# Optimization experiments

Measured on AMD Instinct MI355X. Metric: run time of the kernel, lower is better.

Reference implementation:

```python
import jax, jax.numpy as jnp
import numpy as np

NUM_CLASSES = 21
THRESHOLD = 0.5
VAR0, VAR1 = 0.1, 0.2
NEGPOS_RATIO = 3


def setup_inputs() -> dict:
    key = jax.random.key(0)
    k1, k2, k3, k4, k5, k6, k7 = jax.random.split(key, 7)
    B, P, C, O = 64, 8732, 21, 8
    loc_data = jax.random.normal(k1, (B, P, 4), dtype=jnp.float32) * 0.1
    conf_data = jax.random.normal(k2, (B, P, C), dtype=jnp.float32)
    # priors: center form (cx, cy, w, h), valid in [0,1]
    cxy = jax.random.uniform(k3, (P, 2), minval=0.05, maxval=0.95)
    pwh = jax.random.uniform(k4, (P, 2), minval=0.05, maxval=0.3)
    priors = jnp.concatenate([cxy, pwh], axis=-1).astype(jnp.float32)
    # targets: corner-form boxes + class label (float), (B, O, 5)
    tc = jax.random.uniform(k5, (B, O, 2), minval=0.2, maxval=0.8)
    twh = jax.random.uniform(k6, (B, O, 2), minval=0.1, maxval=0.4)
    tmin = jnp.clip(tc - twh / 2, 0.0, 1.0)
    tmax = jnp.clip(tc + twh / 2, 0.0, 1.0)
    labels = jax.random.randint(k7, (B, O, 1), 0, C - 1).astype(jnp.float32)
    targets = jnp.concatenate([tmin, tmax, labels], axis=-1)
    return {"loc_data": loc_data, "conf_data": conf_data, "priors": priors, "targets": targets}


def _point_form(p):
    # (cx,cy,w,h) -> (xmin,ymin,xmax,ymax)
    return jnp.concatenate([p[:, :2] - p[:, 2:] / 2, p[:, :2] + p[:, 2:] / 2], axis=-1)


def _jaccard(a, b):
    # a: (O,4) corners, b: (P,4) corners -> (O,P)
    lt = jnp.maximum(a[:, None, :2], b[None, :, :2])
    rb = jnp.minimum(a[:, None, 2:], b[None, :, 2:])
    wh = jnp.clip(rb - lt, 0.0, None)
    inter = wh[..., 0] * wh[..., 1]
    area_a = ((a[:, 2] - a[:, 0]) * (a[:, 3] - a[:, 1]))[:, None]
    area_b = ((b[:, 2] - b[:, 0]) * (b[:, 3] - b[:, 1]))[None, :]
    return inter / (area_a + area_b - inter)


def _match_one(truths, labels, priors_pt, priors):
    # truths: (O,4) corners, labels: (O,), priors: (P,4) center-form
    ov = _jaccard(truths, priors_pt)                      # (O,P)
    best_prior_idx = jnp.argmax(ov, axis=1)               # (O,)
    best_truth_overlap = jnp.max(ov, axis=0)              # (P,)
    best_truth_idx = jnp.argmax(ov, axis=0)               # (P,)
    # ensure every gt box matches its best prior
    best_truth_overlap = best_truth_overlap.at[best_prior_idx].set(2.0)
    best_truth_idx = best_truth_idx.at[best_prior_idx].set(jnp.arange(truths.shape[0]))
    matched = truths[best_truth_idx]                      # (P,4)
    conf = labels[best_truth_idx].astype(jnp.int32) + 1
    conf = jnp.where(best_truth_overlap < THRESHOLD, 0, conf)
    # encode offsets
    g_cxcy = ((matched[:, :2] + matched[:, 2:]) / 2 - priors[:, :2]) / (VAR0 * priors[:, 2:])
    g_wh = jnp.log(jnp.clip((matched[:, 2:] - matched[:, :2]) / priors[:, 2:], 1e-8, None)) / VAR1
    return jnp.concatenate([g_cxcy, g_wh], axis=-1), conf


def _forward(loc_data, conf_data, priors, targets):
    B, P, C = conf_data.shape
    priors_sg = jax.lax.stop_gradient(priors)             # torch uses .data
    targets_sg = jax.lax.stop_gradient(targets)
    priors_pt = _point_form(priors_sg)
    loc_t, conf_t = jax.vmap(_match_one, in_axes=(0, 0, None, None))(
        targets_sg[:, :, :4], targets_sg[:, :, 4], priors_pt, priors_sg)
    pos = conf_t > 0                                      # (B,P)

    # localization: smooth L1 summed over positive priors
    diff = loc_data - loc_t
    ad = jnp.abs(diff)
    sl1 = jnp.where(ad < 1.0, 0.5 * diff * diff, ad - 0.5)
    loss_l = jnp.sum(sl1 * pos[..., None].astype(sl1.dtype))

    # per-prior conf loss for hard negative mining
    lse = jax.nn.logsumexp(conf_data, axis=-1)            # (B,P)
    gathered = jnp.take_along_axis(conf_data, conf_t[..., None], axis=-1)[..., 0]
    loss_c_all = lse - gathered                           # (B,P)
    mined = jnp.where(pos, 0.0, loss_c_all)
    loss_idx = jnp.argsort(-mined, axis=1)                # descending
    idx_rank = jnp.argsort(loss_idx, axis=1)
    num_pos = jnp.sum(pos.astype(jnp.int32), axis=1, keepdims=True)  # (B,1)
    num_neg = jnp.minimum(NEGPOS_RATIO * num_pos, P - num_pos)
    neg = idx_rank < num_neg                              # (B,P)

    sel = (pos | neg).astype(loss_c_all.dtype)
    loss_c = jnp.sum(loss_c_all * sel)

    N = jnp.sum(num_pos).astype(loss_l.dtype)
    return loss_l / N, loss_c / N


def reference(loc_data, conf_data, priors, targets):
    return _forward(loc_data, conf_data, priors, targets)
```

## Files before the change

### kernel.cpp

```cpp
#include <hip/hip_runtime.h>
#include <math.h>

#define TPB 256
#define TPBS 1024
#define NVREG 9

typedef unsigned long long ull;
typedef float pf4 __attribute__((ext_vector_type(4), aligned(4)));

__device__ __forceinline__ float jac(float tx0, float ty0, float tx1, float ty1, float ta,
                                     float px0, float py0, float px1, float py1, float pa) {
    float ltx = fmaxf(tx0, px0), lty = fmaxf(ty0, py0);
    float rbx = fminf(tx1, px1), rby = fminf(ty1, py1);
    float w = fmaxf(rbx - ltx, 0.0f), h = fmaxf(rby - lty, 0.0f);
    float inter = w * h;
    return inter / (ta + pa - inter);
}

template <int ON, int CN>
__global__ __launch_bounds__(TPB) void fused_kernel(
    const float* __restrict__ loc, const float* __restrict__ priors,
    const float* __restrict__ targets, const float* __restrict__ conf,
    int P, int O_rt, int C_rt, int CB2,
    float* __restrict__ mined, ull* __restrict__ pkeys,
    float* __restrict__ part_ll, float* __restrict__ part_pc,
    int* __restrict__ part_np, unsigned* __restrict__ chist) {
    constexpr int OMAX = (ON > 0) ? ON : 64;
    constexpr int CC = (CN > 0) ? CN : 32;
    constexpr int WPB = TPB / 64;
    const int O = (ON > 0) ? ON : O_rt;
    const int C = (CN > 0) ? CN : C_rt;
    const int b = blockIdx.x / CB2;
    const int chunk = blockIdx.x % CB2;
    const int tid = threadIdx.x;
    const int p = chunk * TPB + tid;
    const bool pv = (p < P);
    const int lane = tid & 63, wv = tid >> 6;
    const int CB2W = CB2 * WPB;

    __shared__ float s_tx0[OMAX], s_ty0[OMAX], s_tx1[OMAX], s_ty1[OMAX];
    __shared__ float s_lab[OMAX], s_area[OMAX];
    __shared__ int s_h[256];
    __shared__ float s_wll[WPB], s_wpc[WPB];
    __shared__ int s_wnp[WPB];

    float rv[CC];
    float4 pr4 = make_float4(0.f, 0.f, 1.f, 1.f);
    if (pv) {
        const float* row = conf + ((size_t)b * P + p) * C;
        if (CN > 0) {
#pragma unroll
            for (int q = 0; q < CN / 4; ++q) {
                pf4 v = *(const pf4*)(row + 4 * q);
#pragma unroll
                for (int e = 0; e < 4; ++e) rv[4 * q + e] = v[e];
            }
#pragma unroll
            for (int j = (CN / 4) * 4; j < CN; ++j) rv[j] = row[j];
        } else {
            for (int j = 0; j < C; ++j) rv[j] = row[j];
        }
        pr4 = ((const float4*)priors)[p];
    }

    s_h[tid] = 0;
    for (int o = tid; o < O; o += TPB) {
        const float* t = targets + ((size_t)b * O + o) * 5;
        float x0 = t[0], y0 = t[1], x1 = t[2], y1 = t[3];
        s_tx0[o] = x0; s_ty0[o] = y0; s_tx1[o] = x1; s_ty1[o] = y1;
        s_lab[o] = t[4];
        s_area[o] = (x1 - x0) * (y1 - y0);
    }
    __syncthreads();

    float cx = pr4.x, cy = pr4.y, pw = pr4.z, ph = pr4.w;
    float px0 = cx - pw * 0.5f, py0 = cy - ph * 0.5f;
    float px1 = cx + pw * 0.5f, py1 = cy + ph * 0.5f;
    float pa = (px1 - px0) * (py1 - py0);
    float bto = -1.0f;
    int bti = 0;
    for (int o = 0; o < O; ++o) {
        float ov = -1.0f;
        if (pv) {
            ov = jac(s_tx0[o], s_ty0[o], s_tx1[o], s_ty1[o], s_area[o],
                     px0, py0, px1, py1, pa);
            if (ov > bto) { bto = ov; bti = o; }
        }
        float mx = ov;
#pragma unroll
        for (int d = 1; d < 64; d <<= 1)
            mx = fmaxf(mx, __shfl_xor(mx, d, 64));
        ull kk = 0ull;
        if (mx >= 0.0f) {
            ull msk = __ballot(ov == mx);
            int src = __ffsll(msk) - 1;
            unsigned pw_ = (unsigned)(chunk * TPB + (wv << 6) + src);
            kk = ((ull)__float_as_uint(mx) << 32) | (ull)(0xFFFFFFFFu - pw_);
        }
        if (lane == 0)
            pkeys[((size_t)b * O + o) * CB2W + chunk * WPB + wv] = kk;
    }

    float ll = 0.0f, pc = 0.0f;
    int np = 0;
    int bin = 0;
    bool hv = false;
    if (pv) {
        float m = rv[0];
#pragma unroll
        for (int j = 1; j < CC; ++j) { if (CN > 0 || j < C) m = fmaxf(m, rv[j]); }
        float s = 0.0f;
#pragma unroll
        for (int j = 0; j < CC; ++j) { if (CN > 0 || j < C) s += __expf(rv[j] - m); }
        float lse = m + __logf(s);

        int c = (bto < 0.5f) ? 0 : ((int)s_lab[bti] + 1);
        float rowc = rv[0];
#pragma unroll
        for (int j = 1; j < CC; ++j) { if (CN > 0 || j < C) { if (c == j) rowc = rv[j]; } }
        float lc = lse - rowc;

        bool pos = c > 0;
        float mv = pos ? 0.0f : lc;
        mined[(size_t)b * P + p] = mv;
        bin = (int)(__float_as_uint(mv) >> 24);
        hv = true;
        if (pos) {
            pc = lc;
            np = 1;
            float mx0 = s_tx0[bti], my0 = s_ty0[bti];
            float mx1 = s_tx1[bti], my1 = s_ty1[bti];
            float g0 = ((mx0 + mx1) * 0.5f - cx) / (0.1f * pw);
            float g1 = ((my0 + my1) * 0.5f - cy) / (0.1f * ph);
            float g2 = logf(fmaxf((mx1 - mx0) / pw, 1e-8f)) / 0.2f;
            float g3 = logf(fmaxf((my1 - my0) / ph, 1e-8f)) / 0.2f;
            float4 ld = ((const float4*)loc)[(size_t)b * P + p];
            float gt4[4] = {g0, g1, g2, g3};
            float lv[4] = {ld.x, ld.y, ld.z, ld.w};
#pragma unroll
            for (int q = 0; q < 4; ++q) {
                float d = lv[q] - gt4[q];
                float ad = fabsf(d);
                ll += (ad < 1.0f) ? 0.5f * d * d : (ad - 0.5f);
            }
        }
    }

    {
        ull act = __ballot(hv);
        while (act) {
            int src = __ffsll(act) - 1;
            int b0 = __shfl(bin, src, 64);
            ull same = __ballot(hv && bin == b0) & act;
            if (lane == src) atomicAdd(&s_h[b0], (int)__popcll(same));
            act &= ~same;
        }
    }

#pragma unroll
    for (int d = 1; d < 64; d <<= 1) {
        ll += __shfl_xor(ll, d, 64);
        pc += __shfl_xor(pc, d, 64);
        np += __shfl_xor(np, d, 64);
    }
    if (lane == 0) { s_wll[wv] = ll; s_wpc[wv] = pc; s_wnp[wv] = np; }
    __syncthreads();
    if (tid == 0) {
        float L = 0.f, Pc = 0.f;
        int N = 0;
        for (int w = 0; w < WPB; ++w) { L += s_wll[w]; Pc += s_wpc[w]; N += s_wnp[w]; }
        part_ll[blockIdx.x] = L;
        part_pc[blockIdx.x] = Pc;
        part_np[blockIdx.x] = N;
    }
    if (tid < 128) {
        unsigned wd = (unsigned)s_h[2 * tid] | ((unsigned)s_h[2 * tid + 1] << 16);
        chist[((size_t)b * CB2 + chunk) * 128 + tid] = wd;
    }
}

template <int ON, int CN>
__global__ __launch_bounds__(TPBS) void select_kernel(
    const float* __restrict__ mined, const float* __restrict__ conf,
    const float* __restrict__ loc, const float* __restrict__ priors,
    const float* __restrict__ targets, const ull* __restrict__ pkeys,
    const float* __restrict__ part_ll, const float* __restrict__ part_pc,
    const int* __restrict__ part_np, const unsigned* __restrict__ chist,
    float* __restrict__ ll_batch, float* __restrict__ lc_batch,
    int* __restrict__ np_batch,
    int P, int O_rt, int C_rt, int CB2, int ratio) {
    constexpr int OMAX = (ON > 0) ? ON : 64;
    constexpr int NV = NVREG;
    const int O = (ON > 0) ? ON : O_rt;
    const int C = (CN > 0) ? CN : C_rt;
    const int b = blockIdx.x, tid = threadIdx.x;
    const int lane = tid & 63, wv = tid >> 6;
    constexpr int W = TPBS / 64;
    const int CB2W = CB2 * (TPB / 64);
    const float* v = mined + (size_t)b * P;
    const bool reg = (P <= NV * TPBS);

    __shared__ int s_hist[256];
    __shared__ float s_tx0[OMAX], s_ty0[OMAX], s_tx1[OMAX], s_ty1[OMAX];
    __shared__ float s_lab[OMAX], s_area[OMAX];
    __shared__ ull s_keys[OMAX];
    __shared__ int s_bp[OMAX];
    __shared__ float s_wf[W], s_wg[W];
    __shared__ int s_wi[W];
    __shared__ int s_wt[4];
    __shared__ unsigned s_bsel;
    __shared__ int s_krn;
    __shared__ float s_bc[2], s_fix[2];
    __shared__ int s_bn, s_fixn;

    float val[NV];
#pragma unroll
    for (int j = 0; j < NV; ++j) {
        int i = tid + j * TPBS;
        val[j] = (reg && i < P) ? v[i] : 0.0f;
    }

    float pll = 0.0f, ppc = 0.0f;
    int pnp = 0;
    for (int i = tid; i < CB2; i += TPBS) {
        pll += part_ll[b * CB2 + i];
        ppc += part_pc[b * CB2 + i];
        pnp += part_np[b * CB2 + i];
    }
#pragma unroll
    for (int d = 1; d < 64; d <<= 1) {
        pll += __shfl_xor(pll, d, 64);
        ppc += __shfl_xor(ppc, d, 64);
        pnp += __shfl_xor(pnp, d, 64);
    }
    if (lane == 0) { s_wf[wv] = pll; s_wg[wv] = ppc; s_wi[wv] = pnp; }

    if (tid < O) {
        const float* t = targets + ((size_t)b * O + tid) * 5;
        float x0 = t[0], y0 = t[1], x1 = t[2], y1 = t[3];
        s_tx0[tid] = x0; s_ty0[tid] = y0; s_tx1[tid] = x1; s_ty1[tid] = y1;
        s_lab[tid] = t[4];
        s_area[tid] = (x1 - x0) * (y1 - y0);
        s_keys[tid] = 0ull;
    }
    __syncthreads();

    for (int i = tid; i < O * CB2W; i += TPBS) {
        int o = i / CB2W, s = i % CB2W;
        atomicMax(&s_keys[o], pkeys[((size_t)b * O + o) * CB2W + s]);
    }
    __syncthreads();
    if (tid < O)
        s_bp[tid] = (int)(0xFFFFFFFFu - (unsigned)(s_keys[tid] & 0xFFFFFFFFull));
    __syncthreads();

    if (reg) {
#pragma unroll
        for (int j = 0; j < NV; ++j) {
            int i = tid + j * TPBS;
            bool z = false;
            for (int o = 0; o < O; ++o) z |= (s_bp[o] == i);
            if (z) val[j] = 0.0f;
        }
    }
    unsigned uvv[NV];
#pragma unroll
    for (int j = 0; j < NV; ++j) uvv[j] = __float_as_uint(val[j]);

    if (tid < 256) {
        int h = 0;
        const unsigned* cb = chist + (size_t)b * CB2 * 128 + (tid >> 1);
        const int sh = (tid & 1) * 16;
        for (int c = 0; c < CB2; ++c) h += (int)((cb[c * 128] >> sh) & 0xFFFFu);
        s_hist[tid] = h;
    }

    float dll = 0.0f, dpc = 0.0f;
    int dnp = 0;
    int adj_bin = -1;
    if (tid < O) {
        const int o = tid;
        const int p = s_bp[o];
        bool owner = true;
        for (int o2 = o + 1; o2 < O; ++o2)
            if (s_bp[o2] == p) owner = false;
        if (owner) {
            adj_bin = (int)(__float_as_uint(v[p]) >> 24);
            float4 pr = ((const float4*)priors)[p];
            float cx = pr.x, cy = pr.y, pw = pr.z, ph = pr.w;
            float px0 = cx - pw * 0.5f, py0 = cy - ph * 0.5f;
            float px1 = cx + pw * 0.5f, py1 = cy + ph * 0.5f;
            float pa = (px1 - px0) * (py1 - py0);
            float bto = -1.0f;
            int bti = 0;
            for (int o2 = 0; o2 < O; ++o2) {
                float ov = jac(s_tx0[o2], s_ty0[o2], s_tx1[o2], s_ty1[o2], s_area[o2],
                               px0, py0, px1, py1, pa);
                if (ov > bto) { bto = ov; bti = o2; }
            }
            int c_t = (bto < 0.5f) ? 0 : ((int)s_lab[bti] + 1);
            const float* row = conf + ((size_t)b * P + p) * C;
            float m = row[0];
            for (int j = 1; j < C; ++j) m = fmaxf(m, row[j]);
            float s = 0.0f;
            for (int j = 0; j < C; ++j) s += __expf(row[j] - m);
            float lse = m + __logf(s);
            int c_n = (int)s_lab[o] + 1;
            float lc_n = lse - row[c_n];
            bool pos_t = c_t > 0;
            float lc_t = lse - row[c_t];
            dpc = lc_n - (pos_t ? lc_t : 0.0f);
            dnp = 1 - (pos_t ? 1 : 0);
            float4 ld = ((const float4*)loc)[(size_t)b * P + p];
            float lv[4] = {ld.x, ld.y, ld.z, ld.w};
            float sl_new = 0.0f, sl_old = 0.0f;
            {
                float mx0 = s_tx0[o], my0 = s_ty0[o], mx1 = s_tx1[o], my1 = s_ty1[o];
                float g[4] = {((mx0 + mx1) * 0.5f - cx) / (0.1f * pw),
                              ((my0 + my1) * 0.5f - cy) / (0.1f * ph),
                              logf(fmaxf((mx1 - mx0) / pw, 1e-8f)) / 0.2f,
                              logf(fmaxf((my1 - my0) / ph, 1e-8f)) / 0.2f};
                for (int q = 0; q < 4; ++q) {
                    float d = lv[q] - g[q];
                    float ad = fabsf(d);
                    sl_new += (ad < 1.0f) ? 0.5f * d * d : (ad - 0.5f);
                }
            }
            if (pos_t) {
                float mx0 = s_tx0[bti], my0 = s_ty0[bti], mx1 = s_tx1[bti], my1 = s_ty1[bti];
                float g[4] = {((mx0 + mx1) * 0.5f - cx) / (0.1f * pw),
                              ((my0 + my1) * 0.5f - cy) / (0.1f * ph),
                              logf(fmaxf((mx1 - mx0) / pw, 1e-8f)) / 0.2f,
                              logf(fmaxf((my1 - my0) / ph, 1e-8f)) / 0.2f};
                for (int q = 0; q < 4; ++q) {
                    float d = lv[q] - g[q];
                    float ad = fabsf(d);
                    sl_old += (ad < 1.0f) ? 0.5f * d * d : (ad - 0.5f);
                }
            }
            dll = sl_new - sl_old;
        }
    }
    if (wv == 0) {
#pragma unroll
        for (int d = 1; d < 64; d <<= 1) {
            dll += __shfl_xor(dll, d, 64);
            dpc += __shfl_xor(dpc, d, 64);
            dnp += __shfl_xor(dnp, d, 64);
        }
        if (lane == 0) { s_fix[0] = dll; s_fix[1] = dpc; s_fixn = dnp; }
    }
    __syncthreads();
    if (adj_bin > 0) {
        atomicAdd(&s_hist[adj_bin], -1);
        atomicAdd(&s_hist[0], 1);
    }
    if (tid == 0) {
        float L = 0.f, Pc = 0.f;
        int N = 0;
        for (int w = 0; w < W; ++w) { L += s_wf[w]; Pc += s_wg[w]; N += s_wi[w]; }
        s_bc[0] = L + s_fix[0]; s_bc[1] = Pc + s_fix[1]; s_bn = N + s_fixn;
    }
    __syncthreads();
    const float ll_sum = s_bc[0];
    const float sum_pos = s_bc[1];
    const int npos = s_bn;

    const int k = min(ratio * npos, P - npos);
    if (tid == 0) {
        ll_batch[b] = ll_sum;
        np_batch[b] = npos;
    }
    if (k <= 0) {
        if (tid == 0) lc_batch[b] = sum_pos;
        return;
    }

    unsigned prefix = 0u;
    int kr = k;
    for (int pass = 0; pass < 4; ++pass) {
        const int shift = 24 - 8 * pass;
        if (pass > 0) {
            const unsigned mask = 0xFFFFFFFFu << (32 - 8 * pass);
            if (tid < 256) s_hist[tid] = 0;
            __syncthreads();
            if (reg) {
#pragma unroll
                for (int j = 0; j < NV; ++j) {
                    int i = tid + j * TPBS;
                    unsigned u = uvv[j];
                    if (i < P && (u & mask) == prefix)
                        atomicAdd(&s_hist[(u >> shift) & 0xFF], 1);
                }
            } else {
                for (int i = tid; i < P; i += TPBS) {
                    float x = v[i];
                    for (int o = 0; o < O; ++o)
                        if (i == s_bp[o]) x = 0.0f;
                    unsigned u = __float_as_uint(x);
                    if ((u & mask) == prefix)
                        atomicAdd(&s_hist[(u >> shift) & 0xFF], 1);
                }
            }
            __syncthreads();
        }
        int sge = 0, h = 0;
        if (tid < 256) {
            h = s_hist[tid];
            int val_ = h;
#pragma unroll
            for (int d = 1; d < 64; d <<= 1) {
                int t = __shfl_down(val_, d, 64);
                if (lane + d < 64) val_ += t;
            }
            if (lane == 0) s_wt[tid >> 6] = val_;
            sge = val_;
        }
        __syncthreads();
        if (tid < 256) {
            for (int w = (tid >> 6) + 1; w < 4; ++w) sge += s_wt[w];
            int sgt = sge - h;
            if (sge >= kr && sgt < kr) {
                s_bsel = (unsigned)tid;
                s_krn = kr - sgt;
            }
        }
        __syncthreads();
        prefix |= s_bsel << shift;
        kr = s_krn;
    }
    const float T = __uint_as_float(prefix);
    float lsum = 0.0f;
    int lcnt = 0;
    if (reg) {
#pragma unroll
        for (int j = 0; j < NV; ++j) {
            int i = tid + j * TPBS;
            if (i < P && val[j] > T) { lsum += val[j]; ++lcnt; }
        }
    } else {
        for (int i = tid; i < P; i += TPBS) {
            float x = v[i];
            for (int o = 0; o < O; ++o)
                if (i == s_bp[o]) x = 0.0f;
            if (x > T) { lsum += x; ++lcnt; }
        }
    }
#pragma unroll
    for (int d = 1; d < 64; d <<= 1) {
        lsum += __shfl_xor(lsum, d, 64);
        lcnt += __shfl_xor(lcnt, d, 64);
    }
    if (lane == 0) { s_wf[wv] = lsum; s_wi[wv] = lcnt; }
    __syncthreads();
    if (tid == 0) {
        float S = 0.f;
        int Cn = 0;
        for (int w = 0; w < W; ++w) { S += s_wf[w]; Cn += s_wi[w]; }
        lc_batch[b] = sum_pos + S + (float)(k - Cn) * T;
    }
}

__global__ __launch_bounds__(TPB) void finalize_kernel(
    const float* __restrict__ ll_batch, const int* __restrict__ np_batch,
    const float* __restrict__ lc_batch, int B, float* __restrict__ out) {
    const int tid = threadIdx.x;
    __shared__ float s_l[TPB], s_c[TPB];
    __shared__ int s_n[TPB];
    float l = 0.0f, c = 0.0f;
    int n = 0;
    for (int i = tid; i < B; i += TPB) {
        l += ll_batch[i];
        c += lc_batch[i];
        n += np_batch[i];
    }
    s_l[tid] = l; s_c[tid] = c; s_n[tid] = n;
    __syncthreads();
    for (int s = TPB / 2; s > 0; s >>= 1) {
        if (tid < s) {
            s_l[tid] += s_l[tid + s];
            s_c[tid] += s_c[tid + s];
            s_n[tid] += s_n[tid + s];
        }
        __syncthreads();
    }
    if (tid == 0) {
        float N = (float)s_n[0];
        out[0] = s_l[0] / N;
        out[1] = s_c[0] / N;
    }
}

extern "C" void kernel_launch(void* const* d_in, const int* in_sizes, int n_in,
                              void* d_out, int out_size, void* d_ws, size_t ws_size,
                              hipStream_t stream) {
    const float* loc = (const float*)d_in[0];
    const float* conf = (const float*)d_in[1];
    const float* priors = (const float*)d_in[2];
    const float* targets = (const float*)d_in[3];

    const int P = in_sizes[2] / 4;
    const int B = in_sizes[0] / (P * 4);
    const int C = in_sizes[1] / (in_sizes[0] / 4);
    const int O = in_sizes[3] / (B * 5);
    const size_t BP = (size_t)B * P;
    const int CB2 = (P + TPB - 1) / TPB;
    const int CB2W = CB2 * (TPB / 64);

    ull* pkeys = (ull*)d_ws;
    float* mined = (float*)(pkeys + (size_t)B * O * CB2W);
    float* part_ll = mined + BP;
    float* part_pc = part_ll + (size_t)B * CB2;
    int* part_np = (int*)(part_pc + (size_t)B * CB2);
    unsigned* chist = (unsigned*)(part_np + (size_t)B * CB2);
    float* ll_batch = (float*)(chist + (size_t)B * CB2 * 128);
    float* lc_batch = ll_batch + B;
    int* np_batch = (int*)(lc_batch + B);

    if (O == 8 && C == 21) {
        fused_kernel<8, 21><<<B * CB2, TPB, 0, stream>>>(
            loc, priors, targets, conf, P, O, C, CB2,
            mined, pkeys, part_ll, part_pc, part_np, chist);
        select_kernel<8, 21><<<B, TPBS, 0, stream>>>(
            mined, conf, loc, priors, targets, pkeys, part_ll, part_pc, part_np,
            chist, ll_batch, lc_batch, np_batch, P, O, C, CB2, 3);
    } else {
        fused_kernel<0, 0><<<B * CB2, TPB, 0, stream>>>(
            loc, priors, targets, conf, P, O, C, CB2,
            mined, pkeys, part_ll, part_pc, part_np, chist);
        select_kernel<0, 0><<<B, TPBS, 0, stream>>>(
            mined, conf, loc, priors, targets, pkeys, part_ll, part_pc, part_np,
            chist, ll_batch, lc_batch, np_batch, P, O, C, CB2, 3);
    }

    finalize_kernel<<<1, TPB, 0, stream>>>(ll_batch, np_batch, lc_batch, B,
                                           (float*)d_out);
}
```

Measured before the change: 117.9 us.

## Process four prior slots per thread with double-buffered conf row loads

Each block of the fused matching kernel now covers four strips of 256 priors, so every thread handles four priors. Each target box is read from shared memory once and reused across all four IoU computations, and the per-slot overlaps are max-reduced before the wave shuffle. Conf rows are loaded into two alternating register buffers so the next row's load overlaps the current row's log-sum-exp. The aim is fewer blocks, less per-block setup and fewer partial records for the select kernel to reduce. The cost is higher register pressure and only about two blocks per CU for a memory-bound pass, which may hurt latency hiding.

New measurement: 116.8 us. No clear change (-0.9%).

```diff
diff --git a/kernel.cpp b/kernel.cpp
--- a/kernel.cpp
+++ b/kernel.cpp
@@ -2,6 +2,7 @@
 #include <math.h>
 
 #define TPB 256
+#define SLOTS 4
 #define TPBS 1024
 #define NVREG 9
 
@@ -33,20 +34,32 @@
     const int b = blockIdx.x / CB2;
     const int chunk = blockIdx.x % CB2;
     const int tid = threadIdx.x;
-    const int p = chunk * TPB + tid;
-    const bool pv = (p < P);
+    const int base = chunk * (TPB * SLOTS);
     const int lane = tid & 63, wv = tid >> 6;
-    const int CB2W = CB2 * WPB;
+    const int CB2P = CB2 * SLOTS;
 
     __shared__ float s_tx0[OMAX], s_ty0[OMAX], s_tx1[OMAX], s_ty1[OMAX];
     __shared__ float s_lab[OMAX], s_area[OMAX];
     __shared__ int s_h[256];
-    __shared__ float s_wll[WPB], s_wpc[WPB];
-    __shared__ int s_wnp[WPB];
-
-    float rv[CC];
-    float4 pr4 = make_float4(0.f, 0.f, 1.f, 1.f);
-    if (pv) {
+    __shared__ float s_wll[WPB][SLOTS], s_wpc[WPB][SLOTS];
+    __shared__ int s_wnp[WPB][SLOTS];
+
+    int p_[SLOTS];
+    bool pv_[SLOTS];
+#pragma unroll
+    for (int s = 0; s < SLOTS; ++s) { p_[s] = base + s * TPB + tid; pv_[s] = p_[s] < P; }
+
+    float px0[SLOTS], py0[SLOTS], px1[SLOTS], py1[SLOTS], pa[SLOTS];
+#pragma unroll
+    for (int s = 0; s < SLOTS; ++s) {
+        float4 pr = pv_[s] ? ((const float4*)priors)[p_[s]] : make_float4(0.f, 0.f, 1.f, 1.f);
+        px0[s] = pr.x - pr.z * 0.5f; py0[s] = pr.y - pr.w * 0.5f;
+        px1[s] = pr.x + pr.z * 0.5f; py1[s] = pr.y + pr.w * 0.5f;
+        pa[s] = (px1[s] - px0[s]) * (py1[s] - py0[s]);
+    }
+
+    float rvA[CC], rvB[CC];
+    auto loadrow = [&](float* rv, int p) {
         const float* row = conf + ((size_t)b * P + p) * C;
         if (CN > 0) {
 #pragma unroll
@@ -60,8 +73,8 @@
         } else {
             for (int j = 0; j < C; ++j) rv[j] = row[j];
         }
-        pr4 = ((const float4*)priors)[p];
-    }
+    };
+    if (pv_[0]) loadrow(rvA, p_[0]);
 
     s_h[tid] = 0;
     for (int o = tid; o < O; o += TPB) {
@@ -73,105 +86,125 @@
     }
     __syncthreads();
 
-    float cx = pr4.x, cy = pr4.y, pw = pr4.z, ph = pr4.w;
-    float px0 = cx - pw * 0.5f, py0 = cy - ph * 0.5f;
-    float px1 = cx + pw * 0.5f, py1 = cy + ph * 0.5f;
-    float pa = (px1 - px0) * (py1 - py0);
-    float bto = -1.0f;
-    int bti = 0;
+    float bto[SLOTS];
+    int bti[SLOTS];
+#pragma unroll
+    for (int s = 0; s < SLOTS; ++s) { bto[s] = -1.0f; bti[s] = 0; }
     for (int o = 0; o < O; ++o) {
-        float ov = -1.0f;
-        if (pv) {
-            ov = jac(s_tx0[o], s_ty0[o], s_tx1[o], s_ty1[o], s_area[o],
-                     px0, py0, px1, py1, pa);
-            if (ov > bto) { bto = ov; bti = o; }
-        }
-        float mx = ov;
+        float tx0 = s_tx0[o], ty0 = s_ty0[o], tx1 = s_tx1[o], ty1 = s_ty1[o], ta = s_area[o];
+        float ov[SLOTS];
+#pragma unroll
+        for (int s = 0; s < SLOTS; ++s) {
+            ov[s] = pv_[s] ? jac(tx0, ty0, tx1, ty1, ta,
+                                 px0[s], py0[s], px1[s], py1[s], pa[s])
+                           : -1.0f;
+            if (ov[s] > bto[s]) { bto[s] = ov[s]; bti[s] = o; }
+        }
+        float mx = fmaxf(fmaxf(ov[0], ov[1]), fmaxf(ov[2], ov[3]));
 #pragma unroll
         for (int d = 1; d < 64; d <<= 1)
             mx = fmaxf(mx, __shfl_xor(mx, d, 64));
         ull kk = 0ull;
         if (mx >= 0.0f) {
-            ull msk = __ballot(ov == mx);
-            int src = __ffsll(msk) - 1;
-            unsigned pw_ = (unsigned)(chunk * TPB + (wv << 6) + src);
+            ull m0 = __ballot(ov[0] == mx);
+            int ss = 0;
+            if (!m0) { m0 = __ballot(ov[1] == mx); ss = 1; }
+            if (!m0) { m0 = __ballot(ov[2] == mx); ss = 2; }
+            if (!m0) { m0 = __ballot(ov[3] == mx); ss = 3; }
+            int src = __ffsll(m0) - 1;
+            unsigned pw_ = (unsigned)(base + ss * TPB + (wv << 6) + src);
             kk = ((ull)__float_as_uint(mx) << 32) | (ull)(0xFFFFFFFFu - pw_);
         }
         if (lane == 0)
-            pkeys[((size_t)b * O + o) * CB2W + chunk * WPB + wv] = kk;
-    }
-
-    float ll = 0.0f, pc = 0.0f;
-    int np = 0;
-    int bin = 0;
-    bool hv = false;
-    if (pv) {
-        float m = rv[0];
-#pragma unroll
-        for (int j = 1; j < CC; ++j) { if (CN > 0 || j < C) m = fmaxf(m, rv[j]); }
-        float s = 0.0f;
-#pragma unroll
-        for (int j = 0; j < CC; ++j) { if (CN > 0 || j < C) s += __expf(rv[j] - m); }
-        float lse = m + __logf(s);
-
-        int c = (bto < 0.5f) ? 0 : ((int)s_lab[bti] + 1);
-        float rowc = rv[0];
-#pragma unroll
-        for (int j = 1; j < CC; ++j) { if (CN > 0 || j < C) { if (c == j) rowc = rv[j]; } }
-        float lc = lse - rowc;
-
-        bool pos = c > 0;
-        float mv = pos ? 0.0f : lc;
-        mined[(size_t)b * P + p] = mv;
-        bin = (int)(__float_as_uint(mv) >> 24);
-        hv = true;
-        if (pos) {
-            pc = lc;
-            np = 1;
-            float mx0 = s_tx0[bti], my0 = s_ty0[bti];
-            float mx1 = s_tx1[bti], my1 = s_ty1[bti];
-            float g0 = ((mx0 + mx1) * 0.5f - cx) / (0.1f * pw);
-            float g1 = ((my0 + my1) * 0.5f - cy) / (0.1f * ph);
-            float g2 = logf(fmaxf((mx1 - mx0) / pw, 1e-8f)) / 0.2f;
-            float g3 = logf(fmaxf((my1 - my0) / ph, 1e-8f)) / 0.2f;
-            float4 ld = ((const float4*)loc)[(size_t)b * P + p];
-            float gt4[4] = {g0, g1, g2, g3};
-            float lv[4] = {ld.x, ld.y, ld.z, ld.w};
-#pragma unroll
-            for (int q = 0; q < 4; ++q) {
-                float d = lv[q] - gt4[q];
-                float ad = fabsf(d);
-                ll += (ad < 1.0f) ? 0.5f * d * d : (ad - 0.5f);
-            }
-        }
-    }
-
-    {
+            pkeys[((size_t)b * O + o) * CB2P + chunk * WPB + wv] = kk;
+    }
+
+    float ll[SLOTS], pc[SLOTS];
+    int np[SLOTS];
+    auto doSlot = [&](int s, float* rv) {
+        ll[s] = 0.0f; pc[s] = 0.0f; np[s] = 0;
+        bool hv = false;
+        int bn = 0;
+        if (pv_[s]) {
+            float m = rv[0];
+#pragma unroll
+            for (int j = 1; j < CC; ++j) { if (CN > 0 || j < C) m = fmaxf(m, rv[j]); }
+            float sm = 0.0f;
+#pragma unroll
+            for (int j = 0; j < CC; ++j) { if (CN > 0 || j < C) sm += __expf(rv[j] - m); }
+            float lse = m + __logf(sm);
+
+            int c = (bto[s] < 0.5f) ? 0 : ((int)s_lab[bti[s]] + 1);
+            float rowc = rv[0];
+#pragma unroll
+            for (int j = 1; j < CC; ++j) { if (CN > 0 || j < C) { if (c == j) rowc = rv[j]; } }
+            float lc = lse - rowc;
+
+            bool pos = c > 0;
+            float mv = pos ? 0.0f : lc;
+            mined[(size_t)b * P + p_[s]] = mv;
+            bn = (int)(__float_as_uint(mv) >> 24);
+            hv = true;
+            if (pos) {
+                pc[s] = lc;
+                np[s] = 1;
+                float4 pr = ((const float4*)priors)[p_[s]];
+                float cx = pr.x, cy = pr.y, pw = pr.z, ph = pr.w;
+                float mx0 = s_tx0[bti[s]], my0 = s_ty0[bti[s]];
+                float mx1 = s_tx1[bti[s]], my1 = s_ty1[bti[s]];
+                float g0 = ((mx0 + mx1) * 0.5f - cx) / (0.1f * pw);
+                float g1 = ((my0 + my1) * 0.5f - cy) / (0.1f * ph);
+                float g2 = logf(fmaxf((mx1 - mx0) / pw, 1e-8f)) / 0.2f;
+                float g3 = logf(fmaxf((my1 - my0) / ph, 1e-8f)) / 0.2f;
+                float4 ld = ((const float4*)loc)[(size_t)b * P + p_[s]];
+                float gt4[4] = {g0, g1, g2, g3};
+                float lv[4] = {ld.x, ld.y, ld.z, ld.w};
+#pragma unroll
+                for (int q = 0; q < 4; ++q) {
+                    float d = lv[q] - gt4[q];
+                    float ad = fabsf(d);
+                    ll[s] += (ad < 1.0f) ? 0.5f * d * d : (ad - 0.5f);
+                }
+            }
+        }
         ull act = __ballot(hv);
         while (act) {
             int src = __ffsll(act) - 1;
-            int b0 = __shfl(bin, src, 64);
-            ull same = __ballot(hv && bin == b0) & act;
+            int b0 = __shfl(bn, src, 64);
+            ull same = __ballot(hv && bn == b0) & act;
             if (lane == src) atomicAdd(&s_h[b0], (int)__popcll(same));
             act &= ~same;
         }
-    }
-
-#pragma unroll
-    for (int d = 1; d < 64; d <<= 1) {
-        ll += __shfl_xor(ll, d, 64);
-        pc += __shfl_xor(pc, d, 64);
-        np += __shfl_xor(np, d, 64);
-    }
-    if (lane == 0) { s_wll[wv] = ll; s_wpc[wv] = pc; s_wnp[wv] = np; }
-    __syncthreads();
-    if (tid == 0) {
+    };
+    if (pv_[1]) loadrow(rvB, p_[1]);
+    doSlot(0, rvA);
+    if (pv_[2]) loadrow(rvA, p_[2]);
+    doSlot(1, rvB);
+    if (pv_[3]) loadrow(rvB, p_[3]);
+    doSlot(2, rvA);
+    doSlot(3, rvB);
+
+#pragma unroll
+    for (int s = 0; s < SLOTS; ++s) {
+        float l = ll[s], q = pc[s];
+        int n = np[s];
+#pragma unroll
+        for (int d = 1; d < 64; d <<= 1) {
+            l += __shfl_xor(l, d, 64);
+            q += __shfl_xor(q, d, 64);
+            n += __shfl_xor(n, d, 64);
+        }
+        if (lane == 0) { s_wll[wv][s] = l; s_wpc[wv][s] = q; s_wnp[wv][s] = n; }
+    }
+    __syncthreads();
+    if (tid < SLOTS) {
         float L = 0.f, Pc = 0.f;
         int N = 0;
-        for (int w = 0; w < WPB; ++w) { L += s_wll[w]; Pc += s_wpc[w]; N += s_wnp[w]; }
-        part_ll[blockIdx.x] = L;
-        part_pc[blockIdx.x] = Pc;
-        part_np[blockIdx.x] = N;
+        for (int w = 0; w < WPB; ++w) { L += s_wll[w][tid]; Pc += s_wpc[w][tid]; N += s_wnp[w][tid]; }
+        int pidx = b * CB2P + chunk * SLOTS + tid;
+        part_ll[pidx] = L;
+        part_pc[pidx] = Pc;
+        part_np[pidx] = N;
     }
     if (tid < 128) {
         unsigned wd = (unsigned)s_h[2 * tid] | ((unsigned)s_h[2 * tid + 1] << 16);
@@ -196,7 +229,7 @@
     const int b = blockIdx.x, tid = threadIdx.x;
     const int lane = tid & 63, wv = tid >> 6;
     constexpr int W = TPBS / 64;
-    const int CB2W = CB2 * (TPB / 64);
+    const int CB2P = CB2 * SLOTS;
     const float* v = mined + (size_t)b * P;
     const bool reg = (P <= NV * TPBS);
 
@@ -222,10 +255,10 @@
 
     float pll = 0.0f, ppc = 0.0f;
     int pnp = 0;
-    for (int i = tid; i < CB2; i += TPBS) {
-        pll += part_ll[b * CB2 + i];
-        ppc += part_pc[b * CB2 + i];
-        pnp += part_np[b * CB2 + i];
+    for (int i = tid; i < CB2P; i += TPBS) {
+        pll += part_ll[b * CB2P + i];
+        ppc += part_pc[b * CB2P + i];
+        pnp += part_np[b * CB2P + i];
     }
 #pragma unroll
     for (int d = 1; d < 64; d <<= 1) {
@@ -245,9 +278,9 @@
     }
     __syncthreads();
 
-    for (int i = tid; i < O * CB2W; i += TPBS) {
-        int o = i / CB2W, s = i % CB2W;
-        atomicMax(&s_keys[o], pkeys[((size_t)b * O + o) * CB2W + s]);
+    for (int i = tid; i < O * CB2P; i += TPBS) {
+        int o = i / CB2P, s = i % CB2P;
+        atomicMax(&s_keys[o], pkeys[((size_t)b * O + o) * CB2P + s]);
     }
     __syncthreads();
     if (tid < O)
@@ -504,15 +537,15 @@
     const int C = in_sizes[1] / (in_sizes[0] / 4);
     const int O = in_sizes[3] / (B * 5);
     const size_t BP = (size_t)B * P;
-    const int CB2 = (P + TPB - 1) / TPB;
-    const int CB2W = CB2 * (TPB / 64);
+    const int CB2 = (P + TPB * SLOTS - 1) / (TPB * SLOTS);
+    const int CB2P = CB2 * SLOTS;
 
     ull* pkeys = (ull*)d_ws;
-    float* mined = (float*)(pkeys + (size_t)B * O * CB2W);
+    float* mined = (float*)(pkeys + (size_t)B * O * CB2P);
     float* part_ll = mined + BP;
-    float* part_pc = part_ll + (size_t)B * CB2;
-    int* part_np = (int*)(part_pc + (size_t)B * CB2);
-    unsigned* chist = (unsigned*)(part_np + (size_t)B * CB2);
+    float* part_pc = part_ll + (size_t)B * CB2P;
+    int* part_np = (int*)(part_pc + (size_t)B * CB2P);
+    unsigned* chist = (unsigned*)(part_np + (size_t)B * CB2P);
     float* ll_batch = (float*)(chist + (size_t)B * CB2 * 128);
     float* lc_batch = ll_batch + B;
     int* np_batch = (int*)(lc_batch + B);
```
